# Performance work log

Measured on AMD Instinct MI355X. Metric: run time of the kernel, lower is better.

Reference implementation:

```python
import jax, jax.numpy as jnp
import numpy as np

N, P, H, W = 4, 16, 384, 384   # batch, stroke samples, canvas rows/cols
K = 8                          # spline knots -> K-1 segments
BH = BW = 64                   # brush sprite size


def setup_inputs() -> dict:
    key = jax.random.key(0)
    ks = jax.random.split(key, 9)
    images = jax.random.uniform(ks[0], (N, 4, H, W), jnp.float32)
    knot_t = jnp.arange(K, dtype=jnp.float32)
    # segment start values a: x,y inside canvas, z (pressure) in (0.2, 1.0]
    xy = jax.random.uniform(ks[1], (N, K - 1, 2), jnp.float32) * 220.0 + 80.0
    z = jax.random.uniform(ks[2], (N, K - 1, 1), jnp.float32) * 0.8 + 0.2
    a = jnp.concatenate([xy, z], axis=-1)
    b = jax.random.normal(ks[3], (N, K - 1, 3), jnp.float32) * jnp.array([30.0, 30.0, 0.1], jnp.float32)
    two_c = jax.random.normal(ks[4], (N, K - 1, 3), jnp.float32) * jnp.array([5.0, 5.0, 0.02], jnp.float32)
    three_d = jax.random.normal(ks[5], (N, K - 1, 3), jnp.float32) * jnp.array([2.0, 2.0, 0.01], jnp.float32)
    colors = jax.random.uniform(ks[6], (N, 4), jnp.float32)
    ts = jnp.sort(jax.random.uniform(ks[7], (P,), jnp.float32) * (K - 1))
    brush = jax.random.uniform(ks[8], (4, BH, BW), jnp.float32)
    return {"images": images, "knot_t": knot_t, "a": a, "b": b, "two_c": two_c,
            "three_d": three_d, "colors": colors, "ts": ts, "brush": brush}


def _spline_eval(knot_t, a, b, two_c, three_d, ts):
    # torchcubicspline NaturalCubicSpline: x(f) = a + b f + (two_c/2) f^2 + (three_d/3) f^3
    idx = jnp.clip(jnp.searchsorted(knot_t, ts, side="right") - 1, 0, knot_t.shape[0] - 2)  # (P,)
    f = (ts - knot_t[idx])[None, :, None]                       # (1,P,1)
    a_, b_, c_, d_ = a[:, idx], b[:, idx], two_c[:, idx], three_d[:, idx]  # (N,P,3)
    q = a_ + (b_ + (c_ / 2.0 + d_ * f / 3.0) * f) * f
    qd = b_ + (c_ + d_ * f) * f
    return q, qd


def _draw_sprite(brush_p, x, y, theta, s):
    # brush_p: (4, BH+2, BW+2) zero-padded sprite; blit at pose (x,y,theta) with scale s -> (4,H,W)
    rows = jnp.arange(H, dtype=jnp.float32)[:, None]
    cols = jnp.arange(W, dtype=jnp.float32)[None, :]
    dx, dy = cols - x, rows - y
    ct, st = jnp.cos(theta), jnp.sin(theta)
    u = (ct * dx + st * dy) / s + (BW - 1) / 2.0 + 1.0   # +1: pad offset
    v = (-st * dx + ct * dy) / s + (BH - 1) / 2.0 + 1.0
    u0, v0 = jnp.floor(u), jnp.floor(v)
    du, dv = u - u0, v - v0
    u0i = jnp.clip(u0.astype(jnp.int32), 0, BW + 1)
    u1i = jnp.clip(u0i + 1, 0, BW + 1)
    v0i = jnp.clip(v0.astype(jnp.int32), 0, BH + 1)
    v1i = jnp.clip(v0i + 1, 0, BH + 1)
    g = lambda vi, ui: brush_p[:, vi, ui]                 # gather -> (4,H,W)
    return (g(v0i, u0i) * (1 - du) * (1 - dv) + g(v0i, u1i) * du * (1 - dv)
            + g(v1i, u0i) * (1 - du) * dv + g(v1i, u1i) * du * dv)


def reference(images, knot_t, a, b, two_c, three_d, colors, ts, brush):
    q, qd = _spline_eval(knot_t, a, b, two_c, three_d, ts)    # (N,P,3)
    x, y = q[..., 0], q[..., 1]
    theta = -jnp.arctan2(qd[..., 1], qd[..., 0])
    s = jnp.clip(q[..., 2], 0.001, 1.0)
    # per-batch colored brush: rgb channels <- color, alpha scaled by color alpha
    rgb = jnp.broadcast_to(colors[:, :3, None, None], (N, 3, BH, BW))
    alpha = jnp.broadcast_to(brush[None, 3:], (N, 1, BH, BW)) * colors[:, 3, None, None, None]
    brush_b = jnp.concatenate([rgb, alpha], axis=1)           # (N,4,BH,BW)
    brush_p = jnp.pad(brush_b, ((0, 0), (0, 0), (1, 1), (1, 1)))  # zero border = transparent outside
    draw = jax.vmap(jax.vmap(_draw_sprite, in_axes=(None, 0, 0, 0, 0)),
                    in_axes=(0, 0, 0, 0, 0))
    sprites = draw(brush_p, x, y, theta, s)                   # (N,P,4,H,W)
    # oil-paint colorspace: subtractive, p = 1 - v (b2p == p2b == 1-x)
    sprites_oil = 1.0 - sprites
    alphas = 1.0 - sprites_oil[:, :, 3:]                      # sprite alpha     (N,P,1,H,W)
    inv = sprites_oil[:, :, 3:]                               # 1 - alpha
    scaled = sprites_oil[:, :, :3] * alphas                   # premultiplied paint
    active = (q[..., 2] > 0)[:, :, None, None, None]          # z > 0 gate per point
    inv = jnp.where(active, inv, 1.0)
    scaled = jnp.where(active, scaled, 0.0)
    # sequential alpha-over vectorized via suffix products:
    # final = img0 * prod_j inv_j + sum_k scaled_k * prod_{j>k} inv_j
    T_incl = jnp.cumprod(inv[:, ::-1], axis=1)[:, ::-1]       # prod_{j>=k}
    T_excl = jnp.concatenate([T_incl[:, 1:], jnp.ones_like(T_incl[:, :1])], axis=1)
    img0 = 1.0 - images[:, :3]                                # b2p of canvas rgb
    final = img0 * T_incl[:, 0] + jnp.sum(scaled * T_excl, axis=1)
    return 1.0 - final                                        # p2b -> (N,3,H,W)
```

## Files before the change

kernel.cpp:

```cpp
#include <hip/hip_runtime.h>
#include <math.h>

#pragma clang fp contract(off)

namespace {
constexpr int P_STR  = 16;
constexpr int K_KNOT = 8;
constexpr int H = 384;
constexpr int W = 384;
constexpr int BH = 64;
constexpr int BW = 64;
constexpr int TW = 32;
constexpr int TH = 8;
constexpr int NTX = W / TW;
constexpr int NTY = H / TH;
constexpr int NTILES = NTX * NTY;
constexpr int BLK_PER_IMG = 288;
constexpr int TILES_PER_BLK = NTILES / BLK_PER_IMG;
constexpr int PAD = 66;
constexpr int LDSP = 67;
constexpr int AFLOATS = 66 * LDSP + 2;
constexpr int PARAM_F = 8;
constexpr int ALPHA_BASE = 512;
}

__device__ __forceinline__ float fdlibm_atanf_plain(float x)
{
#pragma clang fp contract(off)
    const float atanhi0 = 4.6364760399e-01f, atanhi1 = 7.8539812565e-01f,
                atanhi2 = 9.8279368877e-01f, atanhi3 = 1.5707962513e+00f;
    const float atanlo0 = 5.0121582440e-09f, atanlo1 = 3.7748947079e-08f,
                atanlo2 = 3.4473217170e-08f, atanlo3 = 7.5497894159e-08f;
    const float aT0 = 3.3333328366e-01f, aT1 = -1.9999158382e-01f,
                aT2 = 1.4253635705e-01f, aT3 = -1.0648017377e-01f,
                aT4 = 6.1687607318e-02f;
    const float one = 1.0f;

    const int hx = __float_as_int(x);
    const int ix = hx & 0x7fffffff;
    int id;
    if (ix >= 0x4c800000) {
        if (ix > 0x7f800000) return x + x;
        return (hx > 0) ? (atanhi3 + atanlo3) : (-atanhi3 - atanlo3);
    }
    if (ix < 0x3ee00000) {
        if (ix < 0x39800000) return x;
        id = -1;
    } else {
        x = fabsf(x);
        if (ix < 0x3f980000) {
            if (ix < 0x3f300000) {
                id = 0; x = (2.0f * x - one) / (2.0f + x);
            } else {
                id = 1; x = (x - one) / (x + one);
            }
        } else {
            if (ix < 0x401c0000) {
                id = 2; x = (x - 1.5f) / (one + 1.5f * x);
            } else {
                id = 3; x = -1.0f / x;
            }
        }
    }
    const float z = x * x;
    const float w = z * z;
    const float s1 = z * (aT0 + w * (aT2 + w * aT4));
    const float s2 = w * (aT1 + w * aT3);
    if (id < 0) return x - x * (s1 + s2);
    const float ahi = (id == 0) ? atanhi0 : (id == 1) ? atanhi1 : (id == 2) ? atanhi2 : atanhi3;
    const float alo = (id == 0) ? atanlo0 : (id == 1) ? atanlo1 : (id == 2) ? atanlo2 : atanlo3;
    const float zz = ahi - ((x * (s1 + s2) - alo) - x);
    return (hx < 0) ? -zz : zz;
}

__device__ __forceinline__ float fdlibm_atan2f_plain(float y, float x)
{
#pragma clang fp contract(off)
    const float pi_o_2 = 1.5707963705e+00f;
    const float pi_    = 3.1415927410e+00f;
    const float pi_lo  = -8.7422776573e-08f;

    const int hx = __float_as_int(x), hy = __float_as_int(y);
    const int ix = hx & 0x7fffffff, iy = hy & 0x7fffffff;
    if (ix > 0x7f800000 || iy > 0x7f800000) return x + y;
    if (hx == 0x3f800000) return fdlibm_atanf_plain(y);
    int m = ((hy >> 31) & 1) | ((hx >> 30) & 2);

    if (iy == 0) {
        switch (m) {
            case 0: case 1: return y;
            case 2: return pi_;
            default: return -pi_;
        }
    }
    if (ix == 0) return (hy < 0) ? -pi_o_2 : pi_o_2;
    if (ix == 0x7f800000) {
        if (iy == 0x7f800000) {
            switch (m) {
                case 0: return  pi_o_2 * 0.5f;
                case 1: return -pi_o_2 * 0.5f;
                case 2: return  3.0f * pi_o_2 * 0.5f;
                default: return -3.0f * pi_o_2 * 0.5f;
            }
        }
        switch (m) {
            case 0: return 0.0f;
            case 1: return -0.0f;
            case 2: return pi_;
            default: return -pi_;
        }
    }
    if (iy == 0x7f800000) return (hy < 0) ? -pi_o_2 : pi_o_2;

    const int k = (iy - ix) >> 23;
    float z;
    if (k > 26) {
        z = pi_o_2 + 0.5f * pi_lo;
        m &= 1;
    } else if (hx < 0 && k < -26) {
        z = 0.0f;
    } else {
        z = fdlibm_atanf_plain(fabsf(y / x));
    }
    switch (m) {
        case 0: return z;
        case 1: return -z;
        case 2: return pi_ - (z - pi_lo);
        default: return (z - pi_lo) - pi_;
    }
}

__global__ __launch_bounds__(256) void param_kernel(
    const float* __restrict__ knot_t, const float* __restrict__ a_,
    const float* __restrict__ b_,     const float* __restrict__ c2_,
    const float* __restrict__ d3_,    const float* __restrict__ colors,
    const float* __restrict__ ts,     const float* __restrict__ brush,
    float* __restrict__ ws)
{
#pragma clang fp contract(off)
    const int n   = blockIdx.x;
    const int tid = threadIdx.x;

    if (tid < P_STR) {
        const int p = tid;
        const float t = ts[p];
        int ins = 0;
        #pragma unroll
        for (int i = 0; i < K_KNOT; ++i) ins += (knot_t[i] <= t) ? 1 : 0;
        const int idx = min(max(ins - 1, 0), K_KNOT - 2);
        const float f = t - knot_t[idx];

        const int base = (n * (K_KNOT - 1) + idx) * 3;
        const float C3INV = 0.3333333432674408f;
        float q[3], qd[3];
        #pragma unroll
        for (int j = 0; j < 3; ++j) {
            const float aj = a_[base + j], bj = b_[base + j];
            const float cj = c2_[base + j], dj = d3_[base + j];
            const float inner = cj * 0.5f + (dj * f) * C3INV;
            q[j]  = aj + (bj + inner * f) * f;
            qd[j] = bj + (cj + dj * f) * f;
        }
        const float x = q[0], y = q[1], z = q[2];
        const float s = fminf(fmaxf(z, 0.001f), 1.0f);

        const float apos = fdlibm_atan2f_plain(qd[1], qd[0]);
        const float thf  = -apos;
        const float ct_  = (float)cos((double)thf);
        const float st_  = (float)sin((double)thf);

        float* P = ws + (size_t)(n * P_STR + p) * PARAM_F;
        P[0] = x; P[1] = y; P[2] = 1.0f / s;
        P[3] = ct_; P[4] = st_;
        P[5] = (z > 0.0f) ? 1.0f : 0.0f;
        P[6] = 0.0f; P[7] = 0.0f;
    }

    const float c3 = colors[n * 4 + 3];
    float* A = ws + ALPHA_BASE + (size_t)n * AFLOATS;
    for (int i = tid; i < AFLOATS; i += 256) {
        const int v = i / LDSP;
        const int u = i - v * LDSP;
        float val = 0.0f;
        if ((unsigned)(v - 1) < (unsigned)BH && (unsigned)(u - 1) < (unsigned)BW)
            val = brush[3 * BH * BW + (v - 1) * BW + (u - 1)] * c3;
        A[i] = val;
    }
}

__global__ __launch_bounds__(256) void blit_kernel(
    const float* __restrict__ images, const float* __restrict__ colors,
    const float* __restrict__ ws,     float* __restrict__ out)
{
#pragma clang fp contract(off)
    __shared__ float sP[P_STR * PARAM_F];
    __shared__ __align__(8) float s_alpha[AFLOATS];

    const int n   = blockIdx.z;
    const int L   = blockIdx.x;
    const int tid = threadIdx.x;

    if (tid < P_STR * PARAM_F)
        sP[tid] = ws[(size_t)n * P_STR * PARAM_F + tid];
    {
        const float2* src = reinterpret_cast<const float2*>(
            ws + ALPHA_BASE + (size_t)n * AFLOATS);
        float2* dst = reinterpret_cast<float2*>(s_alpha);
        #pragma unroll
        for (int i = 0; i < AFLOATS / 2; i += 256) {
            const int k = i + tid;
            if (k < AFLOATS / 2) dst[k] = src[k];
        }
    }
    __syncthreads();

    const float col0 = colors[n * 4 + 0];
    const float col1 = colors[n * 4 + 1];
    const float col2 = colors[n * 4 + 2];

    const int lane   = tid & 63;
    const int p_lane = lane & 15;
    const size_t hw  = (size_t)H * W;

    #pragma unroll
    for (int tt = 0; tt < TILES_PER_BLK; ++tt) {
        const int t  = L + tt * BLK_PER_IMG;
        const int tx = t % NTX, ty = t / NTX;
        const int c0 = tx * TW, r0 = ty * TH;

        bool keep = false;
        {
            const float* P = sP + p_lane * PARAM_F;
            if (P[5] > 0.0f) {
                const float x = P[0], y = P[1], rs = P[2];
                const float ct = P[3], st = P[4];
                const float cLo = (float)c0, cHi = (float)(c0 + TW - 1);
                const float rLo = (float)r0, rHi = (float)(r0 + TH - 1);
                const float cu = (ct >= 0.0f) ? cLo : cHi;
                const float ru = (st >= 0.0f) ? rLo : rHi;
                const float umin = (ct * (cu - x) + st * (ru - y)) * rs + 32.5f;
                const float cv = (st <= 0.0f) ? cLo : cHi;
                const float rv = (ct >= 0.0f) ? rLo : rHi;
                const float vmin = (-st * (cv - x) + ct * (rv - y)) * rs + 32.5f;
                keep = (umin < 67.0f) && (vmin < 67.0f);
            }
        }
        const unsigned mask =
            (unsigned)(__ballot(keep && (lane < P_STR)) & 0xFFFFull);

        const int r = r0 + (tid >> 5);
        const int c = c0 + (tid & 31);
        const float rf  = (float)r;
        const float cjf = (float)c;

        const size_t pix = (size_t)r * W + c;
        const size_t imgbase = ((size_t)n * 4) * hw + pix;
        float F0 = 1.0f - images[imgbase];
        float F1 = 1.0f - images[imgbase + hw];
        float F2 = 1.0f - images[imgbase + 2 * hw];

        for (int p = 0; p < P_STR; ++p) {
            if (!((mask >> p) & 1u)) continue;
            const float* P = sP + p * PARAM_F;
            const float x  = P[0], y = P[1], rs = P[2];
            const float ct = P[3], st = P[4];
            const float nst = -st;
            const float dy  = rf - y;
            const float tu  = st * dy;
            const float tv  = ct * dy;
            const float dx  = cjf - x;

            float u = (ct * dx + tu) * rs;
            u = u + 31.5f; u = u + 1.0f;
            float v = (nst * dx + tv) * rs;
            v = v + 31.5f; v = v + 1.0f;

            const float u0f = floorf(u), v0f = floorf(v);
            const float du = u - u0f, dv = v - v0f;
            const int ui = (int)u0f, vi = (int)v0f;
            const int u0c = min(max(ui, 0), PAD - 1);
            const int u1c = min(u0c + 1, PAD - 1);
            const int v0c = min(max(vi, 0), PAD - 1);
            const int v1c = min(v0c + 1, PAD - 1);

            const float inu0 = ((unsigned)(u0c - 1) < 64u) ? 1.0f : 0.0f;
            const float inu1 = ((unsigned)(u1c - 1) < 64u) ? 1.0f : 0.0f;
            const float inv0 = ((unsigned)(v0c - 1) < 64u) ? 1.0f : 0.0f;
            const float inv1 = ((unsigned)(v1c - 1) < 64u) ? 1.0f : 0.0f;
            const float mu = inu0 + du * (inu1 - inu0);
            const float mv = inv0 + dv * (inv1 - inv0);
            const float M  = mu * mv;

            const int b0 = v0c * LDSP, b1 = v1c * LDSP;
            const float a00 = s_alpha[b0 + u0c], a01 = s_alpha[b0 + u1c];
            const float a10 = s_alpha[b1 + u0c], a11 = s_alpha[b1 + u1c];
            const float ax0 = a00 + du * (a01 - a00);
            const float ax1 = a10 + du * (a11 - a10);
            const float av  = ax0 + dv * (ax1 - ax0);

            const float inva = 1.0f - av;
            const float am   = av * M;
            F0 = F0 * inva + (av - col0 * am);
            F1 = F1 * inva + (av - col1 * am);
            F2 = F2 * inva + (av - col2 * am);
        }

        const size_t outbase = ((size_t)n * 3) * hw + pix;
        out[outbase]          = 1.0f - F0;
        out[outbase + hw]     = 1.0f - F1;
        out[outbase + 2 * hw] = 1.0f - F2;
    }
}

extern "C" void kernel_launch(void* const* d_in, const int* in_sizes, int n_in,
                              void* d_out, int out_size, void* d_ws, size_t ws_size,
                              hipStream_t stream) {
    (void)in_sizes; (void)n_in; (void)ws_size; (void)out_size;
    const float* images = (const float*)d_in[0];
    const float* knot_t = (const float*)d_in[1];
    const float* a_     = (const float*)d_in[2];
    const float* b_     = (const float*)d_in[3];
    const float* c2_    = (const float*)d_in[4];
    const float* d3_    = (const float*)d_in[5];
    const float* colors = (const float*)d_in[6];
    const float* ts     = (const float*)d_in[7];
    const float* brush  = (const float*)d_in[8];
    float* out = (float*)d_out;
    float* ws  = (float*)d_ws;

    hipLaunchKernelGGL(param_kernel, dim3(4), dim3(256), 0, stream,
                       knot_t, a_, b_, c2_, d3_, colors, ts, brush, ws);
    hipLaunchKernelGGL(blit_kernel, dim3(BLK_PER_IMG, 1, 4), dim3(256), 0, stream,
                       images, colors, ws, out);
}
```

Baseline: 26.01 us.

## Fuse parameter and blit kernels, recomputing stroke params per block

New measurement: 22.15 us. -14.8%, faster.

```diff
diff --git a/kernel.cpp b/kernel.cpp
--- a/kernel.cpp
+++ b/kernel.cpp
@@ -21,7 +21,6 @@
 constexpr int LDSP = 67;
 constexpr int AFLOATS = 66 * LDSP + 2;
 constexpr int PARAM_F = 8;
-constexpr int ALPHA_BASE = 512;
 }
 
 __device__ __forceinline__ float fdlibm_atanf_plain(float x)
@@ -130,16 +129,22 @@
     }
 }
 
-__global__ __launch_bounds__(256) void param_kernel(
-    const float* __restrict__ knot_t, const float* __restrict__ a_,
-    const float* __restrict__ b_,     const float* __restrict__ c2_,
-    const float* __restrict__ d3_,    const float* __restrict__ colors,
-    const float* __restrict__ ts,     const float* __restrict__ brush,
-    float* __restrict__ ws)
+__global__ __launch_bounds__(256) void blit_fused(
+    const float* __restrict__ images, const float* __restrict__ knot_t,
+    const float* __restrict__ a_,     const float* __restrict__ b_,
+    const float* __restrict__ c2_,    const float* __restrict__ d3_,
+    const float* __restrict__ colors, const float* __restrict__ ts,
+    const float* __restrict__ brush,  float* __restrict__ out)
 {
 #pragma clang fp contract(off)
-    const int n   = blockIdx.x;
+    __shared__ float sP[P_STR * PARAM_F];
+    __shared__ __align__(8) float s_alpha[AFLOATS];
+
+    const int n   = blockIdx.z;
+    const int L   = blockIdx.x;
     const int tid = threadIdx.x;
+
+    const float c3 = colors[n * 4 + 3];
 
     if (tid < P_STR) {
         const int p = tid;
@@ -169,47 +174,20 @@
         const float ct_  = (float)cos((double)thf);
         const float st_  = (float)sin((double)thf);
 
-        float* P = ws + (size_t)(n * P_STR + p) * PARAM_F;
+        float* P = sP + p * PARAM_F;
         P[0] = x; P[1] = y; P[2] = 1.0f / s;
         P[3] = ct_; P[4] = st_;
         P[5] = (z > 0.0f) ? 1.0f : 0.0f;
-        P[6] = 0.0f; P[7] = 0.0f;
-    }
-
-    const float c3 = colors[n * 4 + 3];
-    float* A = ws + ALPHA_BASE + (size_t)n * AFLOATS;
-    for (int i = tid; i < AFLOATS; i += 256) {
-        const int v = i / LDSP;
-        const int u = i - v * LDSP;
-        float val = 0.0f;
-        if ((unsigned)(v - 1) < (unsigned)BH && (unsigned)(u - 1) < (unsigned)BW)
-            val = brush[3 * BH * BW + (v - 1) * BW + (u - 1)] * c3;
-        A[i] = val;
-    }
-}
-
-__global__ __launch_bounds__(256) void blit_kernel(
-    const float* __restrict__ images, const float* __restrict__ colors,
-    const float* __restrict__ ws,     float* __restrict__ out)
-{
-#pragma clang fp contract(off)
-    __shared__ float sP[P_STR * PARAM_F];
-    __shared__ __align__(8) float s_alpha[AFLOATS];
-
-    const int n   = blockIdx.z;
-    const int L   = blockIdx.x;
-    const int tid = threadIdx.x;
-
-    if (tid < P_STR * PARAM_F)
-        sP[tid] = ws[(size_t)n * P_STR * PARAM_F + tid];
-    {
-        const float2* src = reinterpret_cast<const float2*>(
-            ws + ALPHA_BASE + (size_t)n * AFLOATS);
-        float2* dst = reinterpret_cast<float2*>(s_alpha);
-        #pragma unroll
-        for (int i = 0; i < AFLOATS / 2; i += 256) {
-            const int k = i + tid;
-            if (k < AFLOATS / 2) dst[k] = src[k];
+    }
+
+    if (tid >= 64) {
+        for (int i = tid - 64; i < AFLOATS; i += 192) {
+            const int v = i / LDSP;
+            const int u = i - v * LDSP;
+            float val = 0.0f;
+            if ((unsigned)(v - 1) < (unsigned)BH && (unsigned)(u - 1) < (unsigned)BW)
+                val = brush[3 * BH * BW + (v - 1) * BW + (u - 1)] * c3;
+            s_alpha[i] = val;
         }
     }
     __syncthreads();
@@ -315,7 +293,7 @@
 extern "C" void kernel_launch(void* const* d_in, const int* in_sizes, int n_in,
                               void* d_out, int out_size, void* d_ws, size_t ws_size,
                               hipStream_t stream) {
-    (void)in_sizes; (void)n_in; (void)ws_size; (void)out_size;
+    (void)in_sizes; (void)n_in; (void)d_ws; (void)ws_size; (void)out_size;
     const float* images = (const float*)d_in[0];
     const float* knot_t = (const float*)d_in[1];
     const float* a_     = (const float*)d_in[2];
@@ -326,10 +304,7 @@
     const float* ts     = (const float*)d_in[7];
     const float* brush  = (const float*)d_in[8];
     float* out = (float*)d_out;
-    float* ws  = (float*)d_ws;
-
-    hipLaunchKernelGGL(param_kernel, dim3(4), dim3(256), 0, stream,
-                       knot_t, a_, b_, c2_, d3_, colors, ts, brush, ws);
-    hipLaunchKernelGGL(blit_kernel, dim3(BLK_PER_IMG, 1, 4), dim3(256), 0, stream,
-                       images, colors, ws, out);
-}
+
+    hipLaunchKernelGGL(blit_fused, dim3(BLK_PER_IMG, 1, 4), dim3(256), 0, stream,
+                       images, knot_t, a_, b_, c2_, d3_, colors, ts, brush, out);
+}
```
